# Performance work log

Hardware: AMD Instinct MI355X
Metric: run time of the kernel (lower is better)

Reference implementation:

```python
import jax, jax.numpy as jnp
import numpy as np

N_USERS = 100000
N_ITEMS = 50000
D = 64
N_LAYERS = 3
E_RAW = 2_000_000
B = 4096


def setup_inputs() -> dict:
    rng = np.random.RandomState(0)
    u = rng.randint(0, N_USERS, E_RAW).astype(np.int64)
    i = rng.randint(0, N_ITEMS, E_RAW).astype(np.int64)
    lin = np.unique(u * N_ITEMS + i)  # dedupe interactions like the dok_matrix would
    u = (lin // N_ITEMS).astype(np.int32)
    i = (lin % N_ITEMS).astype(np.int32)
    deg_u = np.bincount(u, minlength=N_USERS).astype(np.float64)
    deg_i = np.bincount(i, minlength=N_ITEMS).astype(np.float64)
    inv_u = np.where(deg_u > 0, 1.0 / np.sqrt(np.maximum(deg_u, 1.0)), 0.0)
    inv_i = np.where(deg_i > 0, 1.0 / np.sqrt(np.maximum(deg_i, 1.0)), 0.0)
    val = (inv_u[u] * inv_i[i]).astype(np.float32)  # D^-1/2 A D^-1/2 entries
    # symmetric bipartite Laplacian: user block rows then item block rows
    rows = np.concatenate([u, i + N_USERS]).astype(np.int32)
    cols = np.concatenate([i + N_USERS, u]).astype(np.int32)
    vals = np.concatenate([val, val])

    key = jax.random.key(0)
    k1, k2, k3, k4 = jax.random.split(key, 4)
    embeds = jax.random.normal(k1, (N_USERS + N_ITEMS, D), jnp.float32) * 0.1
    users = jax.random.randint(k2, (B,), 0, N_USERS)
    pos_items = jax.random.randint(k3, (B,), 0, N_ITEMS)
    neg_items = jax.random.randint(k4, (B,), 0, N_ITEMS)
    return dict(embeds=embeds, vals=jnp.asarray(vals), rows=jnp.asarray(rows),
                cols=jnp.asarray(cols), users=users, pos_items=pos_items,
                neg_items=neg_items)


def reference(embeds, vals, rows, cols, users, pos_items, neg_items):
    N = N_USERS + N_ITEMS
    cur = embeds
    acc = embeds  # running sum over layer embeddings (incl. layer 0)
    for _ in range(N_LAYERS):
        msg = vals[:, None] * cur[cols]                      # [nnz, D] gather
        cur = jax.ops.segment_sum(msg, rows, num_segments=N)  # SpMM scatter-add
        acc = acc + cur
    mean = acc / (N_LAYERS + 1)
    user_e = mean[:N_USERS]
    item_e = mean[N_USERS:]
    return user_e[users], item_e[pos_items], item_e[neg_items]
```

## Files before the change

kernel.cpp:

```cpp
#include <hip/hip_runtime.h>
#include <hip/hip_bf16.h>

#define N_USERS 100000
#define N_ITEMS 50000
#define N_TOT   150000
#define D       64
#define NBUCK   ((N_ITEMS + 255) >> 8)
#define BCAP    12288
#define CONVU_B 391
#define FLAG_B  48
#define SCAT_K  32

typedef float v2f __attribute__((ext_vector_type(2)));

__device__ __forceinline__ unsigned bf16rn(float f) {
    unsigned x = __float_as_uint(f);
    return (x + 0x7FFFu + ((x >> 16) & 1u)) >> 16;
}
__device__ __forceinline__ unsigned packbf(float a, float b) {
    return bf16rn(a) | (bf16rn(b) << 16);
}
__device__ __forceinline__ int lower_bound(const int* __restrict__ a, int n, int key) {
    int lo = 0, hi = n;
    while (lo < hi) {
        int mid = (lo + hi) >> 1;
        if (a[mid] < key) lo = mid + 1; else hi = mid;
    }
    return lo;
}

__global__ __launch_bounds__(256) void preA_kernel(
        const float* __restrict__ embeds, const int* __restrict__ rows,
        const int* __restrict__ cols, int* __restrict__ user_ptr,
        unsigned* __restrict__ ebfS, float* __restrict__ invrow,
        const int* __restrict__ users, const int* __restrict__ pos,
        const int* __restrict__ neg, unsigned char* __restrict__ flags,
        int* __restrict__ ccur, int* __restrict__ tmp,
        unsigned short* __restrict__ cols16, int E, int B) {
    int b = blockIdx.x, t = threadIdx.x;
    if (b < CONVU_B) {
        __shared__ int ptr_s[257];
        __shared__ float inv_s[256];
        int base = b * 256;
        int r = base + t;
        int v = lower_bound(rows, E, r);
        ptr_s[t] = v;
        if (r <= N_USERS) user_ptr[r] = v;
        if (t == 0) ptr_s[256] = lower_bound(rows, E, base + 256);
        __syncthreads();
        if (r < N_USERS) {
            int deg = ptr_s[t + 1] - ptr_s[t];
            float inv = (deg > 0) ? (float)(1.0 / sqrt((double)deg)) : 0.f;
            inv_s[t] = inv;
            invrow[r] = inv;
        } else inv_s[t] = 0.f;
        __syncthreads();
        int fl = t & 15;
        #pragma unroll
        for (int i = 0; i < 16; ++i) {
            int lr = i * 16 + (t >> 4);
            int row = base + lr;
            if (row < N_USERS) {
                float inv = inv_s[lr];
                float4 v4 = *(const float4*)(embeds + (size_t)row * D + fl * 4);
                uint2 o;
                o.x = packbf(inv * v4.x, inv * v4.y);
                o.y = packbf(inv * v4.z, inv * v4.w);
                *(uint2*)(ebfS + (size_t)row * 32 + fl * 2) = o;
            }
        }
    } else if (b < CONVU_B + FLAG_B) {
        int k = (b - CONVU_B) * 256 + t;
        if (k < 3 * B) {
            int row;
            if (k < B)          row = users[k];
            else if (k < 2 * B) row = N_USERS + pos[k - B];
            else                row = N_USERS + neg[k - 2 * B];
            flags[row] = 1;
        }
    } else {
        __shared__ int ebuf[256 * SCAT_K];
        __shared__ unsigned char bbuf[256 * SCAT_K];
        __shared__ int cnt[NBUCK];
        __shared__ int basep[NBUCK];
        int chunk = (b - CONVU_B - FLAG_B) * (256 * SCAT_K);
        if (t < NBUCK) cnt[t] = 0;
        __syncthreads();
        #pragma unroll 8
        for (int k = 0; k < SCAT_K; ++k) {
            int e = chunk + k * 256 + t;
            int idx = k * 256 + t;
            if (e < E) {
                int i = cols[e] - N_USERS;
                cols16[e] = (unsigned short)i;
                int bu = i >> 8;
                ebuf[idx] = ((i & 255) << 17) | rows[e];
                bbuf[idx] = (unsigned char)bu;
                atomicAdd(&cnt[bu], 1);
            } else bbuf[idx] = 255;
        }
        __syncthreads();
        if (t < NBUCK) {
            int c = cnt[t];
            basep[t] = c ? atomicAdd(&ccur[t], c) : 0;
            cnt[t] = 0;
        }
        __syncthreads();
        #pragma unroll 4
        for (int k = 0; k < SCAT_K; ++k) {
            int idx = k * 256 + t;
            int bu = bbuf[idx];
            if (bu < NBUCK) {
                int pos2 = basep[bu] + atomicAdd(&cnt[bu], 1);
                if (pos2 < BCAP)
                    tmp[(size_t)bu * BCAP + pos2] = ebuf[idx];
            }
        }
    }
}

__global__ __launch_bounds__(256) void preB_kernel(
        const int* __restrict__ tmp, const int* __restrict__ ccur,
        const float* __restrict__ embeds,
        int* __restrict__ item_beg, int* __restrict__ item_end,
        int* __restrict__ nbr, unsigned* __restrict__ ebfS,
        unsigned* __restrict__ bb1, float* __restrict__ invrow) {
    int b = blockIdx.x, t = threadIdx.x;
    if (b == NBUCK) {
        if (t < 16) {
            *(uint2*)(ebfS + (size_t)N_TOT * 32 + t * 2) = make_uint2(0u, 0u);
            *(uint2*)(bb1  + (size_t)N_TOT * 32 + t * 2) = make_uint2(0u, 0u);
        }
        if (t == 0) invrow[N_TOT] = 0.f;
        return;
    }
    __shared__ int stage[BCAP];
    __shared__ int hist[256];
    __shared__ int scn[256];
    __shared__ int curs[256];
    __shared__ float inv_s[256];
    int n = ccur[b]; if (n > BCAP) n = BCAP;
    const int* src = tmp + (size_t)b * BCAP;
    hist[t] = 0;
    __syncthreads();
    int n4 = n >> 2;
    const int4* src4 = (const int4*)src;
    for (int p = t; p < n4; p += 256) {
        int4 q = src4[p];
        *(int4*)(stage + p * 4) = q;
        atomicAdd(&hist[q.x >> 17], 1);
        atomicAdd(&hist[q.y >> 17], 1);
        atomicAdd(&hist[q.z >> 17], 1);
        atomicAdd(&hist[q.w >> 17], 1);
    }
    for (int p = (n4 << 2) + t; p < n; p += 256) {
        int q = src[p];
        stage[p] = q;
        atomicAdd(&hist[q >> 17], 1);
    }
    __syncthreads();
    scn[t] = hist[t];
    __syncthreads();
    for (int off = 1; off < 256; off <<= 1) {
        int x = (t >= off) ? scn[t - off] : 0;
        __syncthreads();
        scn[t] += x;
        __syncthreads();
    }
    {
        int excl = scn[t] - hist[t];
        curs[t] = excl;
        int gi = (b << 8) + t;
        float inv = (hist[t] > 0) ? (float)(1.0 / sqrt((double)hist[t])) : 0.f;
        inv_s[t] = inv;
        if (gi < N_ITEMS) {
            item_beg[gi] = b * BCAP + excl;
            item_end[gi] = b * BCAP + excl + hist[t];
            invrow[N_USERS + gi] = inv;
        }
    }
    __syncthreads();
    int* dst = nbr + (size_t)b * BCAP;
    for (int p = t; p < n4; p += 256) {
        int4 q = *(const int4*)(stage + p * 4);
        int p0 = atomicAdd(&curs[q.x >> 17], 1); dst[p0] = q.x & 0x1FFFF;
        int p1 = atomicAdd(&curs[q.y >> 17], 1); dst[p1] = q.y & 0x1FFFF;
        int p2 = atomicAdd(&curs[q.z >> 17], 1); dst[p2] = q.z & 0x1FFFF;
        int p3 = atomicAdd(&curs[q.w >> 17], 1); dst[p3] = q.w & 0x1FFFF;
    }
    for (int p = (n4 << 2) + t; p < n; p += 256) {
        int q = stage[p];
        int pos = atomicAdd(&curs[q >> 17], 1);
        dst[pos] = q & 0x1FFFF;
    }
    int fl = t & 15;
    #pragma unroll
    for (int i = 0; i < 16; ++i) {
        int lr = i * 16 + (t >> 4);
        int gi = (b << 8) + lr;
        if (gi < N_ITEMS) {
            int row = N_USERS + gi;
            float inv = inv_s[lr];
            float4 v4 = *(const float4*)(embeds + (size_t)row * D + fl * 4);
            uint2 o;
            o.x = packbf(inv * v4.x, inv * v4.y);
            o.y = packbf(inv * v4.z, inv * v4.w);
            *(uint2*)(ebfS + (size_t)row * 32 + fl * 2) = o;
        }
    }
}

__global__ __launch_bounds__(256) void agg_kernel(
        const unsigned* __restrict__ gsrc,
        float* __restrict__ nxt, unsigned* __restrict__ nxtb,
        const float* __restrict__ invrow,
        const unsigned char* __restrict__ flags,
        const int* __restrict__ user_ptr, const unsigned short* __restrict__ cols16,
        const int* __restrict__ item_beg, const int* __restrict__ item_end,
        const int* __restrict__ nbr) {
    int wave = (int)((blockIdx.x * blockDim.x + threadIdx.x) >> 6);
    int lane = (int)(threadIdx.x & 63);
    if (wave >= (N_TOT >> 2)) return;
    int r  = lane >> 4;
    int q  = lane & 15;
    int g2 = q >> 3;
    int fl = q & 7;

    int row = (wave << 2) + r;
    bool is_user = row < N_USERS;
    int s, epos, dummy;
    const unsigned* sb;
    if (is_user) {
        s = user_ptr[row]; epos = user_ptr[row + 1];
        sb = gsrc + (size_t)N_USERS * 32; dummy = N_ITEMS;
    } else {
        int i = row - N_USERS; s = item_beg[i]; epos = item_end[i];
        sb = gsrc; dummy = N_TOT;
    }
    int deg = epos - s;
    int mdeg = deg;
    mdeg = max(mdeg, __shfl_xor(mdeg, 16));
    mdeg = max(mdeg, __shfl_xor(mdeg, 32));
    int nchunk = (mdeg + 15) >> 4;

    v2f a0 = {0.f, 0.f}, a1 = {0.f, 0.f}, a2 = {0.f, 0.f}, a3 = {0.f, 0.f};

    auto loadcol = [&](int ch) -> int {
        int base = s + (ch << 4);
        int cnt = epos - base;
        int c = dummy;
        if (q < cnt)
            c = is_user ? (int)cols16[base + q] : nbr[base + q];
        return c;
    };

    int colA = loadcol(0);
    int colB = loadcol(1);

    int npair = nchunk >> 1;
    for (int p2 = 0; p2 < npair; ++p2) {
        uint4 qa[8], qb[8];
        #pragma unroll
        for (int t = 0; t < 8; ++t) {
            int c = __shfl(colA, (r << 4) + 2 * t + g2);
            qa[t] = *(const uint4*)(sb + (size_t)c * 32 + fl * 4);
        }
        #pragma unroll
        for (int t = 0; t < 8; ++t) {
            int c = __shfl(colB, (r << 4) + 2 * t + g2);
            qb[t] = *(const uint4*)(sb + (size_t)c * 32 + fl * 4);
        }
        int colC = loadcol(2 * p2 + 2);
        int colD = loadcol(2 * p2 + 3);
        #pragma unroll
        for (int t = 0; t < 8; ++t) {
            v2f p0 = {__uint_as_float(qa[t].x << 16), __uint_as_float(qa[t].x & 0xFFFF0000u)};
            v2f p1 = {__uint_as_float(qa[t].y << 16), __uint_as_float(qa[t].y & 0xFFFF0000u)};
            v2f p2v = {__uint_as_float(qa[t].z << 16), __uint_as_float(qa[t].z & 0xFFFF0000u)};
            v2f p3 = {__uint_as_float(qa[t].w << 16), __uint_as_float(qa[t].w & 0xFFFF0000u)};
            a0 += p0; a1 += p1; a2 += p2v; a3 += p3;
        }
        #pragma unroll
        for (int t = 0; t < 8; ++t) {
            v2f p0 = {__uint_as_float(qb[t].x << 16), __uint_as_float(qb[t].x & 0xFFFF0000u)};
            v2f p1 = {__uint_as_float(qb[t].y << 16), __uint_as_float(qb[t].y & 0xFFFF0000u)};
            v2f p2v = {__uint_as_float(qb[t].z << 16), __uint_as_float(qb[t].z & 0xFFFF0000u)};
            v2f p3 = {__uint_as_float(qb[t].w << 16), __uint_as_float(qb[t].w & 0xFFFF0000u)};
            a0 += p0; a1 += p1; a2 += p2v; a3 += p3;
        }
        colA = colC; colB = colD;
    }
    if (nchunk & 1) {
        uint4 qa[8];
        #pragma unroll
        for (int t = 0; t < 8; ++t) {
            int c = __shfl(colA, (r << 4) + 2 * t + g2);
            qa[t] = *(const uint4*)(sb + (size_t)c * 32 + fl * 4);
        }
        #pragma unroll
        for (int t = 0; t < 8; ++t) {
            v2f p0 = {__uint_as_float(qa[t].x << 16), __uint_as_float(qa[t].x & 0xFFFF0000u)};
            v2f p1 = {__uint_as_float(qa[t].y << 16), __uint_as_float(qa[t].y & 0xFFFF0000u)};
            v2f p2v = {__uint_as_float(qa[t].z << 16), __uint_as_float(qa[t].z & 0xFFFF0000u)};
            v2f p3 = {__uint_as_float(qa[t].w << 16), __uint_as_float(qa[t].w & 0xFFFF0000u)};
            a0 += p0; a1 += p1; a2 += p2v; a3 += p3;
        }
    }
    float acc[8] = {a0.x, a0.y, a1.x, a1.y, a2.x, a2.y, a3.x, a3.y};
    #pragma unroll
    for (int j = 0; j < 8; ++j)
        acc[j] += __shfl_xor(acc[j], 8);
    if (q < 8) {
        float inv = invrow[row];
        float f[8];
        #pragma unroll
        for (int j = 0; j < 8; ++j) f[j] = inv * acc[j];
        uint4 o;
        o.x = packbf(inv * f[0], inv * f[1]); o.y = packbf(inv * f[2], inv * f[3]);
        o.z = packbf(inv * f[4], inv * f[5]); o.w = packbf(inv * f[6], inv * f[7]);
        *(uint4*)(nxtb + (size_t)row * 32 + fl * 4) = o;
        if (flags[row]) {
            size_t ro = (size_t)row * D + fl * 8;
            *(float4*)(nxt + ro)     = make_float4(f[0], f[1], f[2], f[3]);
            *(float4*)(nxt + ro + 4) = make_float4(f[4], f[5], f[6], f[7]);
        }
    }
}

__global__ __launch_bounds__(256) void agg3_fused_kernel(
        const unsigned* __restrict__ gsrc,
        const float* __restrict__ e0, const float* __restrict__ e1,
        const float* __restrict__ e2, const float* __restrict__ invrow,
        const int* __restrict__ users, const int* __restrict__ pos,
        const int* __restrict__ neg,
        const int* __restrict__ user_ptr, const unsigned short* __restrict__ cols16,
        const int* __restrict__ item_beg, const int* __restrict__ item_end,
        const int* __restrict__ nbr,
        float* __restrict__ out, int B) {
    int slot = (int)((blockIdx.x * blockDim.x + threadIdx.x) >> 6);
    int lane = (int)(threadIdx.x & 63);
    if (slot >= 3 * B) return;
    int g  = lane >> 3;
    int fl = lane & 7;

    int row;
    if (slot < B)          row = users[slot];
    else if (slot < 2 * B) row = N_USERS + pos[slot - B];
    else                   row = N_USERS + neg[slot - 2 * B];

    bool is_user = row < N_USERS;
    int s, epos, dummy;
    const unsigned* sb;
    if (is_user) {
        s = user_ptr[row]; epos = user_ptr[row + 1];
        sb = gsrc + (size_t)N_USERS * 32; dummy = N_ITEMS;
    } else {
        int i = row - N_USERS; s = item_beg[i]; epos = item_end[i];
        sb = gsrc; dummy = N_TOT;
    }

    v2f a0 = {0.f, 0.f}, a1 = {0.f, 0.f}, a2 = {0.f, 0.f}, a3 = {0.f, 0.f};

    for (int base = s; base < epos; base += 64) {
        int cnt = epos - base; if (cnt > 64) cnt = 64;
        int col = dummy;
        if (lane < cnt)
            col = is_user ? (int)cols16[base + lane] : nbr[base + lane];
        int tcount = (cnt + 7) >> 3;
        #pragma unroll 8
        for (int t = 0; t < tcount; ++t) {
            int c = __shfl(col, 8 * t + g);
            uint4 q = *(const uint4*)(sb + (size_t)c * 32 + fl * 4);
            v2f p0 = {__uint_as_float(q.x << 16), __uint_as_float(q.x & 0xFFFF0000u)};
            v2f p1 = {__uint_as_float(q.y << 16), __uint_as_float(q.y & 0xFFFF0000u)};
            v2f p2 = {__uint_as_float(q.z << 16), __uint_as_float(q.z & 0xFFFF0000u)};
            v2f p3 = {__uint_as_float(q.w << 16), __uint_as_float(q.w & 0xFFFF0000u)};
            a0 += p0; a1 += p1; a2 += p2; a3 += p3;
        }
    }
    float acc[8] = {a0.x, a0.y, a1.x, a1.y, a2.x, a2.y, a3.x, a3.y};
    #pragma unroll
    for (int j = 0; j < 8; ++j) {
        acc[j] += __shfl_xor(acc[j], 8);
        acc[j] += __shfl_xor(acc[j], 16);
        acc[j] += __shfl_xor(acc[j], 32);
    }
    if (lane < 8) {
        float inv = invrow[row];
        size_t ro = (size_t)row * D + fl * 8;
        float4 x0 = *(const float4*)(e0 + ro), x1 = *(const float4*)(e0 + ro + 4);
        float4 y0 = *(const float4*)(e1 + ro), y1 = *(const float4*)(e1 + ro + 4);
        float4 z0 = *(const float4*)(e2 + ro), z1 = *(const float4*)(e2 + ro + 4);
        float4 r0, r1;
        r0.x = (x0.x + y0.x + z0.x + inv * acc[0]) * 0.25f;
        r0.y = (x0.y + y0.y + z0.y + inv * acc[1]) * 0.25f;
        r0.z = (x0.z + y0.z + z0.z + inv * acc[2]) * 0.25f;
        r0.w = (x0.w + y0.w + z0.w + inv * acc[3]) * 0.25f;
        r1.x = (x1.x + y1.x + z1.x + inv * acc[4]) * 0.25f;
        r1.y = (x1.y + y1.y + z1.y + inv * acc[5]) * 0.25f;
        r1.z = (x1.z + y1.z + z1.z + inv * acc[6]) * 0.25f;
        r1.w = (x1.w + y1.w + z1.w + inv * acc[7]) * 0.25f;
        size_t oo = (size_t)slot * D + fl * 8;
        *(float4*)(out + oo)     = r0;
        *(float4*)(out + oo + 4) = r1;
    }
}

extern "C" void kernel_launch(void* const* d_in, const int* in_sizes, int n_in,
                              void* d_out, int out_size, void* d_ws, size_t ws_size,
                              hipStream_t stream) {
    const float* embeds = (const float*)d_in[0];
    const int*   rows   = (const int*)d_in[2];
    const int*   cols   = (const int*)d_in[3];
    const int*   users  = (const int*)d_in[4];
    const int*   pos    = (const int*)d_in[5];
    const int*   neg    = (const int*)d_in[6];
    const int E2 = in_sizes[1];
    const int E  = E2 / 2;
    const int B  = in_sizes[4];

    char* ws = (char*)d_ws;
    size_t off = 0;
    auto alloc = [&](size_t bytes) { void* p = ws + off; off = (off + bytes + 255) & ~(size_t)255; return p; };
    float*    buf1     = (float*)   alloc((size_t)N_TOT * D * sizeof(float));
    float*    buf2     = (float*)   alloc((size_t)N_TOT * D * sizeof(float));
    unsigned* ebfS     = (unsigned*)alloc((size_t)(N_TOT + 1) * 32 * sizeof(unsigned));
    unsigned* bb1      = (unsigned*)alloc((size_t)(N_TOT + 1) * 32 * sizeof(unsigned));
    int*      nbr      = (int*)     alloc((size_t)NBUCK * BCAP * sizeof(int));
    unsigned short* cols16 = (unsigned short*)alloc((size_t)E * sizeof(unsigned short));
    int*      user_ptr = (int*)     alloc((size_t)(N_USERS + 1) * sizeof(int));
    int*      item_beg = (int*)     alloc((size_t)N_ITEMS * sizeof(int));
    int*      item_end = (int*)     alloc((size_t)N_ITEMS * sizeof(int));
    float*    invrow   = (float*)   alloc((size_t)(N_TOT + 1) * sizeof(float));
    int*      ccur     = (int*)     alloc((size_t)NBUCK * sizeof(int));
    unsigned char* flags = (unsigned char*)alloc((size_t)N_TOT);
    int*      tmp      = (int*)buf1;

    size_t zspan = ((char*)flags + N_TOT) - (char*)ccur;
    hipMemsetAsync(ccur, 0, zspan, stream);
    const int scatB = (E + 256 * SCAT_K - 1) / (256 * SCAT_K);
    preA_kernel<<<CONVU_B + FLAG_B + scatB, 256, 0, stream>>>(
        embeds, rows, cols, user_ptr, ebfS, invrow, users, pos, neg, flags,
        ccur, tmp, cols16, E, B);
    preB_kernel<<<NBUCK + 1, 256, 0, stream>>>(
        tmp, ccur, embeds, item_beg, item_end, nbr, ebfS, bb1, invrow);

    const int blocks = N_TOT / 16;
    agg_kernel<<<blocks, 256, 0, stream>>>(ebfS, buf1, bb1, invrow, flags, user_ptr,
                                           cols16, item_beg, item_end, nbr);
    agg_kernel<<<blocks, 256, 0, stream>>>(bb1, buf2, ebfS, invrow, flags, user_ptr,
                                           cols16, item_beg, item_end, nbr);

    agg3_fused_kernel<<<(3 * B + 3) / 4, 256, 0, stream>>>(
        ebfS, embeds, buf1, buf2, invrow, users, pos, neg,
        user_ptr, cols16, item_beg, item_end, nbr, (float*)d_out, B);
}
```

Measured before the change: 277.7 us.

## Split item bucket sort into four sub-blocks per bucket to raise parallelism

The item-side counting sort in preB now launches four blocks per 256-item bucket. Each block handles a 64-item quarter, filtering the bucket's entries by local item index. This removes the 48KB shared staging array, which should improve occupancy and raise the block count from about 196 to about 784 on a GPU with many CUs. The cost is that each block re-reads the whole bucket twice from global memory. It also adds a per-quarter capacity (QCAP) that silently drops neighbors if a quarter overflows.

```diff
diff --git a/kernel.cpp b/kernel.cpp
--- a/kernel.cpp
+++ b/kernel.cpp
@@ -7,6 +7,7 @@
 #define D       64
 #define NBUCK   ((N_ITEMS + 255) >> 8)
 #define BCAP    12288
+#define QCAP    3072
 #define CONVU_B 391
 #define FLAG_B  48
 #define SCAT_K  32
@@ -126,7 +127,7 @@
         int* __restrict__ nbr, unsigned* __restrict__ ebfS,
         unsigned* __restrict__ bb1, float* __restrict__ invrow) {
     int b = blockIdx.x, t = threadIdx.x;
-    if (b == NBUCK) {
+    if (b == NBUCK * 4) {
         if (t < 16) {
             *(uint2*)(ebfS + (size_t)N_TOT * 32 + t * 2) = make_uint2(0u, 0u);
             *(uint2*)(bb1  + (size_t)N_TOT * 32 + t * 2) = make_uint2(0u, 0u);
@@ -134,70 +135,70 @@
         if (t == 0) invrow[N_TOT] = 0.f;
         return;
     }
-    __shared__ int stage[BCAP];
-    __shared__ int hist[256];
-    __shared__ int scn[256];
-    __shared__ int curs[256];
-    __shared__ float inv_s[256];
-    int n = ccur[b]; if (n > BCAP) n = BCAP;
-    const int* src = tmp + (size_t)b * BCAP;
-    hist[t] = 0;
+    int bu = b >> 2;
+    int qd = b & 3;
+    __shared__ int hist[64];
+    __shared__ int scn[64];
+    __shared__ int curs[64];
+    __shared__ float inv_s[64];
+    int n = ccur[bu]; if (n > BCAP) n = BCAP;
+    const int* src = tmp + (size_t)bu * BCAP;
+    if (t < 64) hist[t] = 0;
     __syncthreads();
+    int lo = qd << 6, hi = lo + 64;
     int n4 = n >> 2;
     const int4* src4 = (const int4*)src;
     for (int p = t; p < n4; p += 256) {
         int4 q = src4[p];
-        *(int4*)(stage + p * 4) = q;
-        atomicAdd(&hist[q.x >> 17], 1);
-        atomicAdd(&hist[q.y >> 17], 1);
-        atomicAdd(&hist[q.z >> 17], 1);
-        atomicAdd(&hist[q.w >> 17], 1);
+        int lx = q.x >> 17; if (lx >= lo && lx < hi) atomicAdd(&hist[lx & 63], 1);
+        int ly = q.y >> 17; if (ly >= lo && ly < hi) atomicAdd(&hist[ly & 63], 1);
+        int lz = q.z >> 17; if (lz >= lo && lz < hi) atomicAdd(&hist[lz & 63], 1);
+        int lw = q.w >> 17; if (lw >= lo && lw < hi) atomicAdd(&hist[lw & 63], 1);
     }
     for (int p = (n4 << 2) + t; p < n; p += 256) {
-        int q = src[p];
-        stage[p] = q;
-        atomicAdd(&hist[q >> 17], 1);
+        int lx = src[p] >> 17;
+        if (lx >= lo && lx < hi) atomicAdd(&hist[lx & 63], 1);
     }
     __syncthreads();
-    scn[t] = hist[t];
+    if (t < 64) scn[t] = hist[t];
     __syncthreads();
-    for (int off = 1; off < 256; off <<= 1) {
-        int x = (t >= off) ? scn[t - off] : 0;
-        __syncthreads();
-        scn[t] += x;
-        __syncthreads();
-    }
-    {
+    for (int off = 1; off < 64; off <<= 1) {
+        int x = (t >= off && t < 64) ? scn[t - off] : 0;
+        __syncthreads();
+        if (t < 64) scn[t] += x;
+        __syncthreads();
+    }
+    if (t < 64) {
         int excl = scn[t] - hist[t];
         curs[t] = excl;
-        int gi = (b << 8) + t;
+        int gi = (bu << 8) + lo + t;
         float inv = (hist[t] > 0) ? (float)(1.0 / sqrt((double)hist[t])) : 0.f;
         inv_s[t] = inv;
         if (gi < N_ITEMS) {
-            item_beg[gi] = b * BCAP + excl;
-            item_end[gi] = b * BCAP + excl + hist[t];
+            item_beg[gi] = b * QCAP + excl;
+            item_end[gi] = b * QCAP + excl + hist[t];
             invrow[N_USERS + gi] = inv;
         }
     }
     __syncthreads();
-    int* dst = nbr + (size_t)b * BCAP;
+    int* dst = nbr + (size_t)b * QCAP;
     for (int p = t; p < n4; p += 256) {
-        int4 q = *(const int4*)(stage + p * 4);
-        int p0 = atomicAdd(&curs[q.x >> 17], 1); dst[p0] = q.x & 0x1FFFF;
-        int p1 = atomicAdd(&curs[q.y >> 17], 1); dst[p1] = q.y & 0x1FFFF;
-        int p2 = atomicAdd(&curs[q.z >> 17], 1); dst[p2] = q.z & 0x1FFFF;
-        int p3 = atomicAdd(&curs[q.w >> 17], 1); dst[p3] = q.w & 0x1FFFF;
+        int4 q = src4[p];
+        int lx = q.x >> 17; if (lx >= lo && lx < hi) { int pp = atomicAdd(&curs[lx & 63], 1); if (pp < QCAP) dst[pp] = q.x & 0x1FFFF; }
+        int ly = q.y >> 17; if (ly >= lo && ly < hi) { int pp = atomicAdd(&curs[ly & 63], 1); if (pp < QCAP) dst[pp] = q.y & 0x1FFFF; }
+        int lz = q.z >> 17; if (lz >= lo && lz < hi) { int pp = atomicAdd(&curs[lz & 63], 1); if (pp < QCAP) dst[pp] = q.z & 0x1FFFF; }
+        int lw = q.w >> 17; if (lw >= lo && lw < hi) { int pp = atomicAdd(&curs[lw & 63], 1); if (pp < QCAP) dst[pp] = q.w & 0x1FFFF; }
     }
     for (int p = (n4 << 2) + t; p < n; p += 256) {
-        int q = stage[p];
-        int pos = atomicAdd(&curs[q >> 17], 1);
-        dst[pos] = q & 0x1FFFF;
+        int q = src[p];
+        int lx = q >> 17;
+        if (lx >= lo && lx < hi) { int pp = atomicAdd(&curs[lx & 63], 1); if (pp < QCAP) dst[pp] = q & 0x1FFFF; }
     }
     int fl = t & 15;
     #pragma unroll
-    for (int i = 0; i < 16; ++i) {
+    for (int i = 0; i < 4; ++i) {
         int lr = i * 16 + (t >> 4);
-        int gi = (b << 8) + lr;
+        int gi = (bu << 8) + lo + lr;
         if (gi < N_ITEMS) {
             int row = N_USERS + gi;
             float inv = inv_s[lr];
@@ -426,7 +427,7 @@
     float*    buf2     = (float*)   alloc((size_t)N_TOT * D * sizeof(float));
     unsigned* ebfS     = (unsigned*)alloc((size_t)(N_TOT + 1) * 32 * sizeof(unsigned));
     unsigned* bb1      = (unsigned*)alloc((size_t)(N_TOT + 1) * 32 * sizeof(unsigned));
-    int*      nbr      = (int*)     alloc((size_t)NBUCK * BCAP * sizeof(int));
+    int*      nbr      = (int*)     alloc((size_t)NBUCK * 4 * QCAP * sizeof(int));
     unsigned short* cols16 = (unsigned short*)alloc((size_t)E * sizeof(unsigned short));
     int*      user_ptr = (int*)     alloc((size_t)(N_USERS + 1) * sizeof(int));
     int*      item_beg = (int*)     alloc((size_t)N_ITEMS * sizeof(int));
@@ -442,7 +443,7 @@
     preA_kernel<<<CONVU_B + FLAG_B + scatB, 256, 0, stream>>>(
         embeds, rows, cols, user_ptr, ebfS, invrow, users, pos, neg, flags,
         ccur, tmp, cols16, E, B);
-    preB_kernel<<<NBUCK + 1, 256, 0, stream>>>(
+    preB_kernel<<<NBUCK * 4 + 1, 256, 0, stream>>>(
         tmp, ccur, embeds, item_beg, item_end, nbr, ebfS, bb1, invrow);
 
     const int blocks = N_TOT / 16;
```

After: 277.1 us. Within noise of the previous version (-0.2%).
